# Performance work log

Hardware: AMD Instinct MI355X
Metric: run time of the kernel (lower is better)

The kernel has to match this reference:

```python
import jax, jax.numpy as jnp
import numpy as np

N, C, H, W = 8, 192, 64, 64
CQK = 24  # C // ratio with ratio=8


def setup_inputs() -> dict:
    key = jax.random.key(0)
    k1, k2, k3, k4 = jax.random.split(key, 4)
    x = jax.random.normal(k1, (N, C, H, W), dtype=jnp.float32)
    Wq = jax.random.normal(k2, (CQK, C), dtype=jnp.float32) * (1.0 / np.sqrt(C))
    Wk = jax.random.normal(k3, (CQK, C), dtype=jnp.float32) * (1.0 / np.sqrt(C))
    Wv = jax.random.normal(k4, (C, C), dtype=jnp.float32) * (1.0 / np.sqrt(C))
    return {"x": x, "Wq": Wq, "Wk": Wk, "Wv": Wv}


def reference(x, Wq, Wk, Wv):
    n, c, h, w = x.shape
    xf = x.reshape(n, c, h * w)                       # [n, C, L]
    q = jnp.einsum('oc,ncl->nol', Wq, xf)             # [n, CQK, L] (1x1 conv)
    k = jnp.einsum('oc,ncl->nol', Wk, xf)             # [n, CQK, L]
    v = jnp.einsum('oc,ncl->nol', Wv, xf)             # [n, C, L]
    # mask[n, l, m] = softmax_m( q[:, :, l] . k[:, :, m] )  -- no scaling in original
    scores = jnp.einsum('nol,nom->nlm', q, k)         # [n, L, L]
    mask = jax.nn.softmax(scores, axis=-1)
    # feat = v @ mask^T : feat[n, c, l] = sum_m v[n, c, m] * mask[n, l, m]
    feat = jnp.einsum('ncm,nlm->ncl', v, mask)
    return feat.reshape(n, c, h, w)
```

## Files before the change

### kernel.cpp

```cpp
#include <hip/hip_runtime.h>
#include <hip/hip_bf16.h>

#define L 4096
#define NB 8
#define C 192
#define CQK 24
#define DP 32
#define QBLK 64
#define KBLK 64
#define NT (L / KBLK)
#define BN 64
#define XS_W 200
#define LOG2E 1.4426950408889634f

typedef _Float16 half_t;
typedef __fp16 fp16x2 __attribute__((ext_vector_type(2)));
typedef __fp16 fp16x4 __attribute__((ext_vector_type(4)));
typedef _Float16 half8 __attribute__((ext_vector_type(8)));
typedef float f32x4 __attribute__((ext_vector_type(4)));


__global__ __launch_bounds__(256, 2) void proj_mfma(const float* __restrict__ x,
                                                    const float* __restrict__ Wq,
                                                    const float* __restrict__ Wk,
                                                    const float* __restrict__ Wv,
                                                    half_t* __restrict__ Qh,
                                                    half_t* __restrict__ Kh,
                                                    half_t* __restrict__ Vh) {
  __shared__ half_t Xs[BN][XS_W];
  __shared__ half_t Qt[BN][DP];
  __shared__ half_t Kt[BN][DP];

  int tid = threadIdx.x;
  int lane = tid & 63;
  int wave = tid >> 6;
  int li = lane & 15;
  int g = lane >> 4;

  int blk = blockIdx.x;
  int n = blk >> 6;
  int l0 = (blk & 63) * BN;

  const float* xbase = x + (size_t)n * C * L + l0;
#pragma unroll
  for (int it = 0; it < 12; ++it) {
    int fid = it * 256 + tid;
    int l4 = fid & 15;
    int c = fid >> 4;
    f32x4 v = *reinterpret_cast<const f32x4*>(xbase + (size_t)c * L + l4 * 4);
#pragma unroll
    for (int j = 0; j < 4; ++j) Xs[l4 * 4 + j][c] = (half_t)v[j];
  }
  __syncthreads();

  const float* rowp[4];
  bool rvalid[4];
#pragma unroll
  for (int mt = 0; mt < 4; ++mt) {
    int row = wave * 64 + mt * 16 + li;
    const float* p;
    bool v = true;
    if (row < 32) {
      v = row < CQK;
      p = Wq + (size_t)(v ? row : 0) * C;
    } else if (row < 64) {
      v = (row - 32) < CQK;
      p = Wk + (size_t)(v ? row - 32 : 0) * C;
    } else {
      p = Wv + (size_t)(row - 64) * C;
    }
    rowp[mt] = p;
    rvalid[mt] = v;
  }

  f32x4 acc[4][4];
#pragma unroll
  for (int mt = 0; mt < 4; ++mt)
#pragma unroll
    for (int nt = 0; nt < 4; ++nt) acc[mt][nt] = {0.f, 0.f, 0.f, 0.f};

  half8 az;
#pragma unroll
  for (int j = 0; j < 8; ++j) az[j] = (half_t)0.f;

#pragma unroll
  for (int kk = 0; kk < 6; ++kk) {
    half8 af[4];
#pragma unroll
    for (int mt = 0; mt < 4; ++mt) {
      const float* p = rowp[mt] + kk * 32 + g * 8;
      f32x4 w0 = *reinterpret_cast<const f32x4*>(p);
      f32x4 w1 = *reinterpret_cast<const f32x4*>(p + 4);
      half8 a;
#pragma unroll
      for (int j = 0; j < 4; ++j) {
        a[j] = (half_t)w0[j];
        a[4 + j] = (half_t)w1[j];
      }
      af[mt] = rvalid[mt] ? a : az;
    }
#pragma unroll
    for (int nt = 0; nt < 4; ++nt) {
      half8 b = *reinterpret_cast<const half8*>(&Xs[nt * 16 + li][kk * 32 + g * 8]);
#pragma unroll
      for (int mt = 0; mt < 4; ++mt)
        acc[mt][nt] = __builtin_amdgcn_mfma_f32_16x16x32_f16(af[mt], b, acc[mt][nt], 0, 0, 0);
    }
  }

  if (wave >= 1) {
#pragma unroll
    for (int mt = 0; mt < 4; ++mt)
#pragma unroll
      for (int nt = 0; nt < 4; ++nt)
#pragma unroll
        for (int r = 0; r < 4; ++r) {
          int c = (wave - 1) * 64 + mt * 16 + 4 * g + r;
          int l = nt * 16 + li;
          Vh[((size_t)n * C + c) * L + l0 + l] = (half_t)acc[mt][nt][r];
        }
  } else {
#pragma unroll
    for (int mt = 0; mt < 4; ++mt)
#pragma unroll
      for (int nt = 0; nt < 4; ++nt)
#pragma unroll
        for (int r = 0; r < 4; ++r) {
          int o = (mt & 1) * 16 + 4 * g + r;
          int l = nt * 16 + li;
          if (mt < 2) Qt[l][o] = (half_t)(acc[mt][nt][r] * LOG2E);
          else        Kt[l][o] = (half_t)acc[mt][nt][r];
        }
  }
  __syncthreads();

  if (tid < 128) {
    int which = tid >> 6;
    int l = tid & 63;
    const half8* src = reinterpret_cast<const half8*>(which ? &Kt[l][0] : &Qt[l][0]);
    half_t* dstp = (which ? Kh : Qh) + ((size_t)n * L + l0 + l) * DP;
    half8* dst = reinterpret_cast<half8*>(dstp);
#pragma unroll
    for (int i = 0; i < 4; ++i) dst[i] = src[i];
  }
}


struct SMemA {
  half_t P[2][QBLK][64];
  float rs[2][QBLK];
  float Ls[QBLK];
};

__global__ __launch_bounds__(256, 2) void attn(const half_t* __restrict__ Qh,
                                               const half_t* __restrict__ Kh,
                                               const half_t* __restrict__ Vh,
                                               float* __restrict__ out) {
  __shared__ SMemA sm;

  const int tid = threadIdx.x;
  const int wave = tid >> 6;
  const int lane = tid & 63;
  const int li = lane & 15;
  const int g = lane >> 4;
  const int n = blockIdx.x;
  const int q0 = blockIdx.y * QBLK;
  const int c0 = wave * 48;
  const int swz = (li & 7) << 4;

  const half8 qfrag = *reinterpret_cast<const half8*>(
      Qh + ((size_t)(n * L + q0 + wave * 16 + li)) * DP + g * 8);

  const char* kptr = (const char*)(Kh + (size_t)n * L * DP) +
                     ((size_t)li * DP + g * 8) * 2;
  const char* vb[3];
  vb[0] = (const char*)(Vh + (size_t)n * C * L) +
          ((size_t)(c0 + li) * L + g * 8) * 2;
  vb[1] = vb[0] + (size_t)16 * L * 2;
  vb[2] = vb[0] + (size_t)32 * L * 2;

  f32x4 acc[3][4];
#pragma unroll
  for (int ct = 0; ct < 3; ++ct)
#pragma unroll
    for (int qt = 0; qt < 4; ++qt) acc[ct][qt] = {0.f, 0.f, 0.f, 0.f};

  float Lrow = 0.f;
  float coff = -28.f;

  half8 kA[4], vA[6], kB[4], vB[6];

  auto sm_write = [&](const f32x4(&s)[4], int par) {
    float p[4][4];
    float mx = -1.0e30f;
#pragma unroll
    for (int b = 0; b < 4; ++b) {
      mx = fmaxf(mx, fmaxf(fmaxf(s[b][0], s[b][1]), fmaxf(s[b][2], s[b][3])));
#pragma unroll
      for (int r = 0; r < 4; ++r) p[b][r] = __builtin_amdgcn_exp2f(s[b][r]);
    }
    float sc = 1.0f;
    if (__any((int)(mx > 15.f))) {
      float m2 = fmaxf(mx, __shfl_xor(mx, 16));
      m2 = fmaxf(m2, __shfl_xor(m2, 32));
      if (m2 > 15.f) {
        sc = __builtin_amdgcn_exp2f(-m2);
        Lrow *= sc;
        coff -= m2;
#pragma unroll
        for (int b = 0; b < 4; ++b)
#pragma unroll
          for (int r = 0; r < 4; ++r)
            p[b][r] = __builtin_amdgcn_exp2f(s[b][r] - m2);
      }
    }
#pragma unroll
    for (int b = 0; b < 4; ++b)
#pragma unroll
      for (int r = 0; r < 4; ++r) Lrow += p[b][r];

    char* prow = (char*)&sm.P[par][wave * 16 + li][0];
#pragma unroll
    for (int b = 0; b < 4; ++b) {
      fp16x2 lo = __builtin_amdgcn_cvt_pkrtz(p[b][0], p[b][1]);
      fp16x2 hi = __builtin_amdgcn_cvt_pkrtz(p[b][2], p[b][3]);
      fp16x4 h = __builtin_shufflevector(lo, hi, 0, 1, 2, 3);
      *reinterpret_cast<fp16x4*>(prow + ((b * 32 + 8 * g) ^ swz)) = h;
    }
    if (lane < 16) sm.rs[par][li * 4 + wave] = sc;
  };

  auto apply_rescale = [&](int par) {
    f32x4 f = *reinterpret_cast<const f32x4*>(&sm.rs[par][li * 4]);
    bool an = (f[0] != 1.f) | (f[1] != 1.f) | (f[2] != 1.f) | (f[3] != 1.f);
    if (__any((int)an)) {
#pragma unroll
      for (int ct = 0; ct < 3; ++ct)
#pragma unroll
        for (int qt = 0; qt < 4; ++qt) acc[ct][qt] *= f[qt];
    }
  };

  auto pv = [&](const half8(&vp)[6], int par) {
#pragma unroll
    for (int ch = 0; ch < 2; ++ch)
#pragma unroll
      for (int qt = 0; qt < 4; ++qt) {
        const char* prow = (const char*)&sm.P[par][qt * 16 + li][0];
        half8 pfrag = *reinterpret_cast<const half8*>(
            prow + ((ch * 64 + 16 * g) ^ swz));
#pragma unroll
        for (int ct = 0; ct < 3; ++ct)
          acc[ct][qt] = __builtin_amdgcn_mfma_f32_16x16x32_f16(
              vp[ct * 2 + ch], pfrag, acc[ct][qt], 0, 0, 0);
      }
  };

#pragma unroll
  for (int b = 0; b < 4; ++b)
    kA[b] = *reinterpret_cast<const half8*>(kptr + b * 1024);
  kptr += KBLK * DP * 2;
#pragma unroll
  for (int b = 0; b < 4; ++b)
    kB[b] = *reinterpret_cast<const half8*>(kptr + b * 1024);
  kptr += KBLK * DP * 2;
#pragma unroll
  for (int ct = 0; ct < 3; ++ct) {
    vA[ct * 2 + 0] = *reinterpret_cast<const half8*>(vb[ct]);
    vA[ct * 2 + 1] = *reinterpret_cast<const half8*>(vb[ct] + 64);
    vb[ct] += KBLK * 2;
  }
  {
    f32x4 cvec = {coff, coff, coff, coff};
    f32x4 s[4];
#pragma unroll
    for (int b = 0; b < 4; ++b)
      s[b] = __builtin_amdgcn_mfma_f32_16x16x32_f16(kA[b], qfrag, cvec, 0, 0, 0);
    sm_write(s, 0);
  }
  asm volatile("s_waitcnt lgkmcnt(0)\n\ts_barrier" ::: "memory");

  auto phase = [&](const half8(&kq)[4], const half8(&vp)[6], half8(&kd)[4],
                   half8(&vd)[6], int par, bool doK) {
    if (doK) {
#pragma unroll
      for (int b = 0; b < 4; ++b)
        kd[b] = *reinterpret_cast<const half8*>(kptr + b * 1024);
      kptr += KBLK * DP * 2;
    }
#pragma unroll
    for (int ct = 0; ct < 3; ++ct) {
      vd[ct * 2 + 0] = *reinterpret_cast<const half8*>(vb[ct]);
      vd[ct * 2 + 1] = *reinterpret_cast<const half8*>(vb[ct] + 64);
      vb[ct] += KBLK * 2;
    }

    f32x4 cvec = {coff, coff, coff, coff};
    f32x4 s[4];
#pragma unroll
    for (int b = 0; b < 4; ++b)
      s[b] = __builtin_amdgcn_mfma_f32_16x16x32_f16(kq[b], qfrag, cvec, 0, 0, 0);

    apply_rescale(par);
    pv(vp, par);

    sm_write(s, par ^ 1);
    asm volatile("s_waitcnt lgkmcnt(0)\n\ts_barrier" ::: "memory");
  };

  for (int t = 0; t < 62; t += 2) {
    phase(kB, vA, kA, vB, 0, true);
    phase(kA, vB, kB, vA, 1, true);
  }
  phase(kB, vA, kA, vB, 0, false);

  apply_rescale(1);
  pv(vB, 1);

  float sum = Lrow;
  sum += __shfl_xor(sum, 16);
  sum += __shfl_xor(sum, 32);
  if (lane < 16) sm.Ls[li * 4 + wave] = sum;
  __syncthreads();

  f32x4 Lv = *reinterpret_cast<const f32x4*>(&sm.Ls[li * 4]);
  float inv[4];
#pragma unroll
  for (int qt = 0; qt < 4; ++qt) inv[qt] = 1.0f / Lv[qt];

#pragma unroll
  for (int ct = 0; ct < 3; ++ct)
#pragma unroll
    for (int qt = 0; qt < 4; ++qt)
#pragma unroll
      for (int r = 0; r < 4; ++r)
        out[((size_t)n * C + c0 + ct * 16 + 4 * g + r) * L + q0 + qt * 16 + li] =
            acc[ct][qt][r] * inv[qt];
}


extern "C" void kernel_launch(void* const* d_in, const int* in_sizes, int n_in,
                              void* d_out, int out_size, void* d_ws, size_t ws_size,
                              hipStream_t stream) {
  (void)in_sizes; (void)n_in; (void)out_size; (void)ws_size;
  const float* x = (const float*)d_in[0];
  const float* Wq = (const float*)d_in[1];
  const float* Wk = (const float*)d_in[2];
  const float* Wv = (const float*)d_in[3];
  float* out = (float*)d_out;

  half_t* Qh = (half_t*)d_ws;
  half_t* Kh = Qh + (size_t)NB * L * DP;
  half_t* Vh = Kh + (size_t)NB * L * DP;

  hipLaunchKernelGGL(proj_mfma, dim3(NB * (L / BN)), dim3(256), 0, stream,
                     x, Wq, Wk, Wv, Qh, Kh, Vh);
  hipLaunchKernelGGL(attn, dim3(NB, L / QBLK), dim3(256), 0, stream,
                     Qh, Kh, Vh, out);
}
```

Baseline: 142.8 us.

## Double key block size and restructure attention pipeline with single register buffers

Raises the key/value tile from 64 to 128 columns per iteration, halving the number of barrier-separated iterations and softmax bookkeeping passes. The K/V double-register ping-pong is replaced by single register sets, with K prefetched right after the score MFMAs and V loaded after the PV MFMAs. MFMA sections are wrapped in s_setprio raises. It risks more register pressure, less load latency hiding because V is fetched just before use, and a larger shared P buffer.

```diff
diff --git a/kernel.cpp b/kernel.cpp
--- a/kernel.cpp
+++ b/kernel.cpp
@@ -7,7 +7,7 @@
 #define CQK 24
 #define DP 32
 #define QBLK 64
-#define KBLK 64
+#define KBLK 128
 #define NT (L / KBLK)
 #define BN 64
 #define XS_W 200
@@ -147,7 +147,7 @@
 
 
 struct SMemA {
-  half_t P[2][QBLK][64];
+  half_t P[2][QBLK][KBLK];
   float rs[2][QBLK];
   float Ls[QBLK];
 };
@@ -188,13 +188,31 @@
   float Lrow = 0.f;
   float coff = -28.f;
 
-  half8 kA[4], vA[6], kB[4], vB[6];
-
-  auto sm_write = [&](const f32x4(&s)[4], int par) {
-    float p[4][4];
+  half8 kreg[8];
+  half8 vreg[12];
+
+  auto loadK = [&]() {
+#pragma unroll
+    for (int b = 0; b < 8; ++b)
+      kreg[b] = *reinterpret_cast<const half8*>(kptr + b * 1024);
+    kptr += KBLK * DP * 2;
+  };
+  auto loadV = [&]() {
+#pragma unroll
+    for (int ct = 0; ct < 3; ++ct)
+#pragma unroll
+      for (int ch = 0; ch < 4; ++ch)
+        vreg[ct * 4 + ch] =
+            *reinterpret_cast<const half8*>(vb[ct] + ch * 64);
+#pragma unroll
+    for (int ct = 0; ct < 3; ++ct) vb[ct] += KBLK * 2;
+  };
+
+  auto sm_write = [&](const f32x4(&s)[8], int par) {
+    float p[8][4];
     float mx = -1.0e30f;
 #pragma unroll
-    for (int b = 0; b < 4; ++b) {
+    for (int b = 0; b < 8; ++b) {
       mx = fmaxf(mx, fmaxf(fmaxf(s[b][0], s[b][1]), fmaxf(s[b][2], s[b][3])));
 #pragma unroll
       for (int r = 0; r < 4; ++r) p[b][r] = __builtin_amdgcn_exp2f(s[b][r]);
@@ -208,20 +226,20 @@
         Lrow *= sc;
         coff -= m2;
 #pragma unroll
-        for (int b = 0; b < 4; ++b)
+        for (int b = 0; b < 8; ++b)
 #pragma unroll
           for (int r = 0; r < 4; ++r)
             p[b][r] = __builtin_amdgcn_exp2f(s[b][r] - m2);
       }
     }
 #pragma unroll
-    for (int b = 0; b < 4; ++b)
+    for (int b = 0; b < 8; ++b)
 #pragma unroll
       for (int r = 0; r < 4; ++r) Lrow += p[b][r];
 
     char* prow = (char*)&sm.P[par][wave * 16 + li][0];
 #pragma unroll
-    for (int b = 0; b < 4; ++b) {
+    for (int b = 0; b < 8; ++b) {
       fp16x2 lo = __builtin_amdgcn_cvt_pkrtz(p[b][0], p[b][1]);
       fp16x2 hi = __builtin_amdgcn_cvt_pkrtz(p[b][2], p[b][3]);
       fp16x4 h = __builtin_shufflevector(lo, hi, 0, 1, 2, 3);
@@ -241,9 +259,10 @@
     }
   };
 
-  auto pv = [&](const half8(&vp)[6], int par) {
-#pragma unroll
-    for (int ch = 0; ch < 2; ++ch)
+  auto pv = [&](int par) {
+    __builtin_amdgcn_s_setprio(1);
+#pragma unroll
+    for (int ch = 0; ch < 4; ++ch)
 #pragma unroll
       for (int qt = 0; qt < 4; ++qt) {
         const char* prow = (const char*)&sm.P[par][qt * 16 + li][0];
@@ -252,70 +271,47 @@
 #pragma unroll
         for (int ct = 0; ct < 3; ++ct)
           acc[ct][qt] = __builtin_amdgcn_mfma_f32_16x16x32_f16(
-              vp[ct * 2 + ch], pfrag, acc[ct][qt], 0, 0, 0);
+              vreg[ct * 4 + ch], pfrag, acc[ct][qt], 0, 0, 0);
       }
-  };
-
-#pragma unroll
-  for (int b = 0; b < 4; ++b)
-    kA[b] = *reinterpret_cast<const half8*>(kptr + b * 1024);
-  kptr += KBLK * DP * 2;
-#pragma unroll
-  for (int b = 0; b < 4; ++b)
-    kB[b] = *reinterpret_cast<const half8*>(kptr + b * 1024);
-  kptr += KBLK * DP * 2;
-#pragma unroll
-  for (int ct = 0; ct < 3; ++ct) {
-    vA[ct * 2 + 0] = *reinterpret_cast<const half8*>(vb[ct]);
-    vA[ct * 2 + 1] = *reinterpret_cast<const half8*>(vb[ct] + 64);
-    vb[ct] += KBLK * 2;
-  }
+    __builtin_amdgcn_s_setprio(0);
+  };
+
+  loadK();
+  loadV();
   {
     f32x4 cvec = {coff, coff, coff, coff};
-    f32x4 s[4];
-#pragma unroll
-    for (int b = 0; b < 4; ++b)
-      s[b] = __builtin_amdgcn_mfma_f32_16x16x32_f16(kA[b], qfrag, cvec, 0, 0, 0);
+    f32x4 s[8];
+    __builtin_amdgcn_s_setprio(1);
+#pragma unroll
+    for (int b = 0; b < 8; ++b)
+      s[b] = __builtin_amdgcn_mfma_f32_16x16x32_f16(kreg[b], qfrag, cvec, 0, 0, 0);
+    __builtin_amdgcn_s_setprio(0);
+    loadK();
     sm_write(s, 0);
   }
   asm volatile("s_waitcnt lgkmcnt(0)\n\ts_barrier" ::: "memory");
 
-  auto phase = [&](const half8(&kq)[4], const half8(&vp)[6], half8(&kd)[4],
-                   half8(&vd)[6], int par, bool doK) {
-    if (doK) {
-#pragma unroll
-      for (int b = 0; b < 4; ++b)
-        kd[b] = *reinterpret_cast<const half8*>(kptr + b * 1024);
-      kptr += KBLK * DP * 2;
-    }
-#pragma unroll
-    for (int ct = 0; ct < 3; ++ct) {
-      vd[ct * 2 + 0] = *reinterpret_cast<const half8*>(vb[ct]);
-      vd[ct * 2 + 1] = *reinterpret_cast<const half8*>(vb[ct] + 64);
-      vb[ct] += KBLK * 2;
-    }
-
+  for (int t = 0; t < NT - 1; ++t) {
+    const int par = t & 1;
     f32x4 cvec = {coff, coff, coff, coff};
-    f32x4 s[4];
-#pragma unroll
-    for (int b = 0; b < 4; ++b)
-      s[b] = __builtin_amdgcn_mfma_f32_16x16x32_f16(kq[b], qfrag, cvec, 0, 0, 0);
+    f32x4 s[8];
+    __builtin_amdgcn_s_setprio(1);
+#pragma unroll
+    for (int b = 0; b < 8; ++b)
+      s[b] = __builtin_amdgcn_mfma_f32_16x16x32_f16(kreg[b], qfrag, cvec, 0, 0, 0);
+    __builtin_amdgcn_s_setprio(0);
+    if (t < NT - 2) loadK();
 
     apply_rescale(par);
-    pv(vp, par);
+    pv(par);
+    loadV();
 
     sm_write(s, par ^ 1);
     asm volatile("s_waitcnt lgkmcnt(0)\n\ts_barrier" ::: "memory");
-  };
-
-  for (int t = 0; t < 62; t += 2) {
-    phase(kB, vA, kA, vB, 0, true);
-    phase(kA, vB, kB, vA, 1, true);
-  }
-  phase(kB, vA, kA, vB, 0, false);
+  }
 
   apply_rescale(1);
-  pv(vB, 1);
+  pv(1);
 
   float sum = Lrow;
   sum += __shfl_xor(sum, 16);
```

After: 143.5 us. About the same (+0.5%).

## Split attention KV range in two with fp16 partials and merge kernel

Applied to the files above, without the earlier changes.

Templates the attention kernel to split the key/value sequence into two halves along a new grid z dimension, doubling the block count from 512 to 1024 and raising the launch-bounds occupancy hint. Each half writes fp16 partial outputs scaled by a power-of-two normaliser, plus row sums and offsets. A new merge kernel combines the two partials in log-sum-exp fashion. It also raises wave priority around the MFMA sections. This adds a third kernel launch, extra workspace traffic for the partials, and fp16 rounding of the unnormalised partials. The old single-pass path remains as a fallback when the workspace is too small.

```diff
diff --git a/kernel.cpp b/kernel.cpp
--- a/kernel.cpp
+++ b/kernel.cpp
@@ -8,7 +8,6 @@
 #define DP 32
 #define QBLK 64
 #define KBLK 64
-#define NT (L / KBLK)
 #define BN 64
 #define XS_W 200
 #define LOG2E 1.4426950408889634f
@@ -147,15 +146,18 @@
 
 
 struct SMemA {
-  half_t P[2][QBLK][64];
+  half_t P[2][QBLK][KBLK];
   float rs[2][QBLK];
   float Ls[QBLK];
+  float Cs[QBLK];
 };
 
-__global__ __launch_bounds__(256, 2) void attn(const half_t* __restrict__ Qh,
-                                               const half_t* __restrict__ Kh,
-                                               const half_t* __restrict__ Vh,
-                                               float* __restrict__ out) {
+template <bool SPLIT2>
+__global__ __launch_bounds__(256, SPLIT2 ? 4 : 2) void attn(
+    const half_t* __restrict__ Qh, const half_t* __restrict__ Kh,
+    const half_t* __restrict__ Vh, float* __restrict__ out,
+    half_t* __restrict__ Op, float* __restrict__ Lp, float* __restrict__ Cp) {
+  constexpr int NTT = (SPLIT2 ? L / 2 : L) / KBLK;
   __shared__ SMemA sm;
 
   const int tid = threadIdx.x;
@@ -165,16 +167,18 @@
   const int g = lane >> 4;
   const int n = blockIdx.x;
   const int q0 = blockIdx.y * QBLK;
+  const int z = blockIdx.z;
+  const int kv0 = z * (SPLIT2 ? L / 2 : 0);
   const int c0 = wave * 48;
   const int swz = (li & 7) << 4;
 
   const half8 qfrag = *reinterpret_cast<const half8*>(
       Qh + ((size_t)(n * L + q0 + wave * 16 + li)) * DP + g * 8);
 
-  const char* kptr = (const char*)(Kh + (size_t)n * L * DP) +
+  const char* kptr = (const char*)(Kh + (size_t)(n * L + kv0) * DP) +
                      ((size_t)li * DP + g * 8) * 2;
   const char* vb[3];
-  vb[0] = (const char*)(Vh + (size_t)n * C * L) +
+  vb[0] = (const char*)(Vh + (size_t)n * C * L + kv0) +
           ((size_t)(c0 + li) * L + g * 8) * 2;
   vb[1] = vb[0] + (size_t)16 * L * 2;
   vb[2] = vb[0] + (size_t)32 * L * 2;
@@ -242,6 +246,7 @@
   };
 
   auto pv = [&](const half8(&vp)[6], int par) {
+    __builtin_amdgcn_s_setprio(1);
 #pragma unroll
     for (int ch = 0; ch < 2; ++ch)
 #pragma unroll
@@ -254,6 +259,7 @@
           acc[ct][qt] = __builtin_amdgcn_mfma_f32_16x16x32_f16(
               vp[ct * 2 + ch], pfrag, acc[ct][qt], 0, 0, 0);
       }
+    __builtin_amdgcn_s_setprio(0);
   };
 
 #pragma unroll
@@ -297,9 +303,11 @@
 
     f32x4 cvec = {coff, coff, coff, coff};
     f32x4 s[4];
+    __builtin_amdgcn_s_setprio(1);
 #pragma unroll
     for (int b = 0; b < 4; ++b)
       s[b] = __builtin_amdgcn_mfma_f32_16x16x32_f16(kq[b], qfrag, cvec, 0, 0, 0);
+    __builtin_amdgcn_s_setprio(0);
 
     apply_rescale(par);
     pv(vp, par);
@@ -308,7 +316,7 @@
     asm volatile("s_waitcnt lgkmcnt(0)\n\ts_barrier" ::: "memory");
   };
 
-  for (int t = 0; t < 62; t += 2) {
+  for (int t = 0; t < NTT - 2; t += 2) {
     phase(kB, vA, kA, vB, 0, true);
     phase(kA, vB, kB, vA, 1, true);
   }
@@ -320,29 +328,84 @@
   float sum = Lrow;
   sum += __shfl_xor(sum, 16);
   sum += __shfl_xor(sum, 32);
-  if (lane < 16) sm.Ls[li * 4 + wave] = sum;
+  if (lane < 16) {
+    sm.Ls[li * 4 + wave] = sum;
+    sm.Cs[li * 4 + wave] = coff;
+  }
   __syncthreads();
 
   f32x4 Lv = *reinterpret_cast<const f32x4*>(&sm.Ls[li * 4]);
-  float inv[4];
-#pragma unroll
-  for (int qt = 0; qt < 4; ++qt) inv[qt] = 1.0f / Lv[qt];
-
-#pragma unroll
-  for (int ct = 0; ct < 3; ++ct)
-#pragma unroll
-    for (int qt = 0; qt < 4; ++qt)
-#pragma unroll
-      for (int r = 0; r < 4; ++r)
-        out[((size_t)n * C + c0 + ct * 16 + 4 * g + r) * L + q0 + qt * 16 + li] =
-            acc[ct][qt][r] * inv[qt];
+
+  if constexpr (!SPLIT2) {
+    float inv[4];
+#pragma unroll
+    for (int qt = 0; qt < 4; ++qt) inv[qt] = 1.0f / Lv[qt];
+#pragma unroll
+    for (int ct = 0; ct < 3; ++ct)
+#pragma unroll
+      for (int qt = 0; qt < 4; ++qt)
+#pragma unroll
+        for (int r = 0; r < 4; ++r)
+          out[((size_t)n * C + c0 + ct * 16 + 4 * g + r) * L + q0 + qt * 16 + li] =
+              acc[ct][qt][r] * inv[qt];
+  } else {
+    f32x4 Cv = *reinterpret_cast<const f32x4*>(&sm.Cs[li * 4]);
+    float osc[4];
+    int eb[4];
+#pragma unroll
+    for (int qt = 0; qt < 4; ++qt) {
+      eb[qt] = (int)(__float_as_uint(Lv[qt]) >> 23) - 127;
+      osc[qt] = __uint_as_float((uint32_t)(127 - eb[qt]) << 23);
+    }
+    half_t* ob = Op + (size_t)(n * 2 + z) * C * L;
+#pragma unroll
+    for (int ct = 0; ct < 3; ++ct)
+#pragma unroll
+      for (int qt = 0; qt < 4; ++qt)
+#pragma unroll
+        for (int r = 0; r < 4; ++r)
+          ob[((size_t)(c0 + ct * 16 + 4 * g + r)) * L + q0 + qt * 16 + li] =
+              (half_t)(acc[ct][qt][r] * osc[qt]);
+    if (lane < 16) {
+      size_t ridx = (size_t)(n * 2 + z) * L + q0 + wave * 16 + li;
+      Lp[ridx] = Lv[wave] * osc[wave];
+      Cp[ridx] = (float)eb[wave] - Cv[wave];
+    }
+  }
+}
+
+
+__global__ __launch_bounds__(256) void merge_split(
+    const half_t* __restrict__ Op, const float* __restrict__ Lp,
+    const float* __restrict__ Cp, float* __restrict__ out) {
+  int n = blockIdx.x;
+  int l = blockIdx.y * 64 + (threadIdx.x & 63);
+  int cs = threadIdx.x >> 6;
+
+  size_t ra = (size_t)(n * 2 + 0) * L + l;
+  size_t rb = (size_t)(n * 2 + 1) * L + l;
+  float La = Lp[ra], Ca = Cp[ra];
+  float Lb = Lp[rb], Cb = Cp[rb];
+  float cm = fmaxf(Ca, Cb);
+  float fa = exp2f(Ca - cm), fb = exp2f(Cb - cm);
+  float D = La * fa + Lb * fb;
+  float wa = fa / D, wb = fb / D;
+
+  const half_t* Oa = Op + (size_t)(n * 2 + 0) * C * L;
+  const half_t* Ob = Op + (size_t)(n * 2 + 1) * C * L;
+  float* ob = out + (size_t)n * C * L;
+#pragma unroll
+  for (int j = 0; j < 48; ++j) {
+    size_t idx = (size_t)(cs * 48 + j) * L + l;
+    ob[idx] = wa * (float)Oa[idx] + wb * (float)Ob[idx];
+  }
 }
 
 
 extern "C" void kernel_launch(void* const* d_in, const int* in_sizes, int n_in,
                               void* d_out, int out_size, void* d_ws, size_t ws_size,
                               hipStream_t stream) {
-  (void)in_sizes; (void)n_in; (void)out_size; (void)ws_size;
+  (void)in_sizes; (void)n_in; (void)out_size;
   const float* x = (const float*)d_in[0];
   const float* Wq = (const float*)d_in[1];
   const float* Wk = (const float*)d_in[2];
@@ -352,9 +415,21 @@
   half_t* Qh = (half_t*)d_ws;
   half_t* Kh = Qh + (size_t)NB * L * DP;
   half_t* Vh = Kh + (size_t)NB * L * DP;
+  half_t* Op = Vh + (size_t)NB * C * L;
+  float* Lp = (float*)(Op + (size_t)NB * 2 * C * L);
+  float* Cp = Lp + (size_t)NB * 2 * L;
+
+  size_t need = (size_t)((char*)(Cp + (size_t)NB * 2 * L) - (char*)d_ws);
 
   hipLaunchKernelGGL(proj_mfma, dim3(NB * (L / BN)), dim3(256), 0, stream,
                      x, Wq, Wk, Wv, Qh, Kh, Vh);
-  hipLaunchKernelGGL(attn, dim3(NB, L / QBLK), dim3(256), 0, stream,
-                     Qh, Kh, Vh, out);
+  if (ws_size >= need) {
+    hipLaunchKernelGGL((attn<true>), dim3(NB, L / QBLK, 2), dim3(256), 0,
+                       stream, Qh, Kh, Vh, out, Op, Lp, Cp);
+    hipLaunchKernelGGL(merge_split, dim3(NB, L / 64), dim3(256), 0, stream,
+                       Op, Lp, Cp, out);
+  } else {
+    hipLaunchKernelGGL((attn<false>), dim3(NB, L / QBLK, 1), dim3(256), 0,
+                       stream, Qh, Kh, Vh, out, Op, Lp, Cp);
+  }
 }
```

New measurement: 368.7 us. 2.58x slower.
